# Kernel optimization log

Hardware: AMD Instinct MI355X
Metric: run time of the kernel (lower is better)

The kernel has to match this reference:

```python
import jax, jax.numpy as jnp
import numpy as np

WINDOW_SIZE = 11
SIGMA = 1.5
CHANNELS = 3
DATA_RANGE = 1.0


def _create_window(window_size, channel):
    x = np.arange(window_size) - window_size // 2
    g = np.exp(-(x ** 2) / (2.0 * SIGMA ** 2))
    g = g / g.sum()
    w2d = np.outer(g, g).astype(np.float32)  # [ws, ws]
    # depthwise kernel, OIHW with I=1, O=channel
    return jnp.asarray(np.broadcast_to(w2d, (channel, 1, window_size, window_size)).copy())


def _depthwise_conv(x, window, channel):
    # x: [B, C, H, W], window: [C, 1, ws, ws], VALID padding, groups=C
    return jax.lax.conv_general_dilated(
        x, window, window_strides=(1, 1), padding='VALID',
        dimension_numbers=('NCHW', 'OIHW', 'NCHW'),
        feature_group_count=channel)


def setup_inputs() -> dict:
    key = jax.random.key(0)
    k1, k2 = jax.random.split(key)
    img1 = jax.random.uniform(k1, (32, CHANNELS, 512, 512), dtype=jnp.float32)
    img2 = jax.random.uniform(k2, (32, CHANNELS, 512, 512), dtype=jnp.float32)
    return {"img1": img1, "img2": img2}


def reference(img1, img2):
    channel = img1.shape[1]
    window = _create_window(WINDOW_SIZE, channel).astype(img1.dtype)

    mu1 = _depthwise_conv(img1, window, channel)
    mu2 = _depthwise_conv(img2, window, channel)
    mu1_sq = mu1 * mu1
    mu2_sq = mu2 * mu2
    mu1_mu2 = mu1 * mu2

    sigma1_sq = _depthwise_conv(img1 * img1, window, channel) - mu1_sq
    sigma2_sq = _depthwise_conv(img2 * img2, window, channel) - mu2_sq
    sigma12 = _depthwise_conv(img1 * img2, window, channel) - mu1_mu2

    C1 = (0.01 * DATA_RANGE) ** 2
    C2 = (0.03 * DATA_RANGE) ** 2
    v1 = 2.0 * sigma12 + C2
    v2 = sigma1_sq + sigma2_sq + C2
    ssim_map = (2.0 * mu1_mu2 + C1) * v1 / ((mu1_sq + mu2_sq + C1) * v2)
    # mean over channel, height, width -> per-image SSIM [B]
    return ssim_map.mean(axis=(1, 2, 3))
```

## Files before the change

kernel.cpp:

```cpp
#include <hip/hip_runtime.h>
#include <math.h>

#define H 512
#define W 512
#define OUT_H 502
#define OUT_W 502
#define C1c 1.0e-4f
#define C2c 9.0e-4f

#define TH 56
#define NR (TH + 10)
#define NCOLS 256
#define HALO 10

__global__ __launch_bounds__(256, 4) void ssim_kernel(const float* __restrict__ img1,
                                                      const float* __restrict__ img2,
                                                      float* __restrict__ out) {
    __shared__ float2 ring[2][NCOLS + HALO];
    __shared__ float wsum[4];

    const int tid = threadIdx.x;

    float g[11];
    {
        float s = 0.f;
#pragma unroll
        for (int i = 0; i < 11; ++i) {
            float d = (float)(i - 5);
            g[i] = expf(-d * d * (1.0f / 4.5f));
            s += g[i];
        }
        float inv = 1.0f / s;
#pragma unroll
        for (int i = 0; i < 11; ++i) g[i] *= inv;
    }

    const int X0 = blockIdx.x * NCOLS;
    const int Y0 = blockIdx.y * TH;
    const int plane = blockIdx.z;
    const size_t pbase = (size_t)plane * (H * W);
    const float* __restrict__ p1 = img1 + pbase;
    const float* __restrict__ p2 = img2 + pbase;

    const int gx = X0 + tid;
    const int hx = min(X0 + NCOLS + tid, W - 1);

    float acc0[11], acc1[11], acc2[11], acc3[11], acc4[11];
#pragma unroll
    for (int i = 0; i < 11; ++i) { acc0[i]=0.f; acc1[i]=0.f; acc2[i]=0.f; acc3[i]=0.f; acc4[i]=0.f; }

    float lsum = 0.f;

    {
        const size_t rowoff = (size_t)min(Y0, H - 1) * W;
    }
    int gy0 = min(Y0, H - 1);
    float a1 = p1[(size_t)gy0 * W + gx];
    float a2 = p2[(size_t)gy0 * W + gx];
    float b1 = 0.f, b2 = 0.f;
    if (tid < HALO) { b1 = p1[(size_t)gy0 * W + hx]; b2 = p2[(size_t)gy0 * W + hx]; }

#pragma unroll 1
    for (int rb = 0; rb < NR; rb += 11) {
#pragma unroll
        for (int p = 0; p < 11; ++p) {
            const int r = rb + p;
            const int slot = r & 1;

            ring[slot][tid] = make_float2(a1, a2);
            if (tid < HALO) ring[slot][NCOLS + tid] = make_float2(b1, b2);

            {
                const int gy = min(Y0 + r + 1, H - 1);
                const size_t rowoff = (size_t)gy * W;
                a1 = p1[rowoff + gx];
                a2 = p2[rowoff + gx];
                if (tid < HALO) { b1 = p1[rowoff + hx]; b2 = p2[rowoff + hx]; }
            }

            __syncthreads();

            float h0 = 0.f, h1 = 0.f, h2 = 0.f, h3 = 0.f, h4 = 0.f;
            const float2* rp = &ring[slot][tid];
#pragma unroll
            for (int t = 0; t < 11; ++t) {
                const float2 v = rp[t];
                const float w = g[t];
                h0 = fmaf(w, v.x,       h0);
                h1 = fmaf(w, v.y,       h1);
                h2 = fmaf(w, v.x * v.x, h2);
                h3 = fmaf(w, v.y * v.y, h3);
                h4 = fmaf(w, v.x * v.y, h4);
            }

#pragma unroll
            for (int a = 0; a < 11; ++a) {
                const float w = g[(p - a + 11) % 11];
                acc0[a] = fmaf(w, h0, acc0[a]);
                acc1[a] = fmaf(w, h1, acc1[a]);
                acc2[a] = fmaf(w, h2, acc2[a]);
                acc3[a] = fmaf(w, h3, acc3[a]);
                acc4[a] = fmaf(w, h4, acc4[a]);
            }

            const int e = (p + 1) % 11;
            if (r >= 10) {
                const int oy = Y0 + r - 10;
                const float m1 = acc0[e], m2 = acc1[e];
                const float m1s = m1 * m1, m2s = m2 * m2, m12 = m1 * m2;
                const float sig1  = acc2[e] - m1s;
                const float sig2  = acc3[e] - m2s;
                const float sig12 = acc4[e] - m12;
                const float num = (2.f * m12 + C1c) * (2.f * sig12 + C2c);
                const float den = (m1s + m2s + C1c) * (sig1 + sig2 + C2c);
                const float v = num * __builtin_amdgcn_rcpf(den);
                if (gx < OUT_W && oy < OUT_H) lsum += v;
            }
            acc0[e] = 0.f; acc1[e] = 0.f; acc2[e] = 0.f; acc3[e] = 0.f; acc4[e] = 0.f;
        }
    }

#pragma unroll
    for (int off = 32; off > 0; off >>= 1) lsum += __shfl_down(lsum, off, 64);
    if ((tid & 63) == 0) wsum[tid >> 6] = lsum;
    __syncthreads();
    if (tid == 0) {
        const float inv_count = 1.0f / (3.0f * (float)OUT_H * (float)OUT_W);
        const float total = (wsum[0] + wsum[1] + wsum[2] + wsum[3]) * inv_count;
        atomicAdd(&out[plane / 3], total);
    }
}

__global__ void zero_out(float* out, int n) {
    int i = threadIdx.x + blockIdx.x * blockDim.x;
    if (i < n) out[i] = 0.f;
}

extern "C" void kernel_launch(void* const* d_in, const int* in_sizes, int n_in,
                              void* d_out, int out_size, void* d_ws, size_t ws_size,
                              hipStream_t stream) {
    const float* img1 = (const float*)d_in[0];
    const float* img2 = (const float*)d_in[1];
    float* out = (float*)d_out;

    zero_out<<<1, 64, 0, stream>>>(out, out_size);

    const int nplanes = in_sizes[0] / (H * W);
    dim3 grid(W / NCOLS,
              (OUT_H + TH - 1) / TH,
              nplanes);
    ssim_kernel<<<grid, 256, 0, stream>>>(img1, img2, out);
}
```

Baseline: 262.3 us.

## Give each wavefront a private 64-column ring, replacing block barriers with wave barriers

```diff
diff --git a/kernel.cpp b/kernel.cpp
--- a/kernel.cpp
+++ b/kernel.cpp
@@ -1,64 +1,58 @@
 #include <hip/hip_runtime.h>
-#include <math.h>
 
 #define H 512
 #define W 512
-#define OUT_H 502
-#define OUT_W 502
+#define OUT_Wc 502
+#define OUT_Hc 502
 #define C1c 1.0e-4f
 #define C2c 9.0e-4f
 
 #define TH 56
-#define NR (TH + 10)
-#define NCOLS 256
+#define NR 66
 #define HALO 10
+#define RSTRIDE 74
 
-__global__ __launch_bounds__(256, 4) void ssim_kernel(const float* __restrict__ img1,
+__global__ __launch_bounds__(256, 5) void ssim_kernel(const float* __restrict__ img1,
                                                       const float* __restrict__ img2,
                                                       float* __restrict__ out) {
-    __shared__ float2 ring[2][NCOLS + HALO];
-    __shared__ float wsum[4];
+    __shared__ float2 ring[4][2][RSTRIDE];
 
-    const int tid = threadIdx.x;
+    constexpr float GW[11] = {0.00102838f, 0.00759876f, 0.03600078f, 0.10936067f,
+                              0.21300555f, 0.26601174f, 0.21300555f, 0.10936067f,
+                              0.03600078f, 0.00759876f, 0.00102838f};
 
-    float g[11];
-    {
-        float s = 0.f;
-#pragma unroll
-        for (int i = 0; i < 11; ++i) {
-            float d = (float)(i - 5);
-            g[i] = expf(-d * d * (1.0f / 4.5f));
-            s += g[i];
-        }
-        float inv = 1.0f / s;
-#pragma unroll
-        for (int i = 0; i < 11; ++i) g[i] *= inv;
-    }
+    const int tid  = threadIdx.x;
+    const int wv   = tid >> 6;
+    const int lane = tid & 63;
 
-    const int X0 = blockIdx.x * NCOLS;
-    const int Y0 = blockIdx.y * TH;
     const int plane = blockIdx.z;
     const size_t pbase = (size_t)plane * (H * W);
     const float* __restrict__ p1 = img1 + pbase;
     const float* __restrict__ p2 = img2 + pbase;
 
-    const int gx = X0 + tid;
-    const int hx = min(X0 + NCOLS + tid, W - 1);
+    const int Y0    = blockIdx.y * TH;
+    const int wcol0 = (blockIdx.x * 4 + wv) * 64;
+    const int gx    = wcol0 + lane;
+    const int hx    = min(wcol0 + 64 + lane, W - 1);
+
+    float2 (* __restrict__ wring)[RSTRIDE] = ring[wv];
 
     float acc0[11], acc1[11], acc2[11], acc3[11], acc4[11];
 #pragma unroll
     for (int i = 0; i < 11; ++i) { acc0[i]=0.f; acc1[i]=0.f; acc2[i]=0.f; acc3[i]=0.f; acc4[i]=0.f; }
 
+    const bool colok = (gx < OUT_Wc);
     float lsum = 0.f;
 
     {
-        const size_t rowoff = (size_t)min(Y0, H - 1) * W;
+        const float* r1 = p1 + (size_t)Y0 * W;
+        const float* r2 = p2 + (size_t)Y0 * W;
     }
-    int gy0 = min(Y0, H - 1);
-    float a1 = p1[(size_t)gy0 * W + gx];
-    float a2 = p2[(size_t)gy0 * W + gx];
+    const float* r1p = p1 + (size_t)Y0 * W;
+    const float* r2p = p2 + (size_t)Y0 * W;
+    float a1 = r1p[gx], a2 = r2p[gx];
     float b1 = 0.f, b2 = 0.f;
-    if (tid < HALO) { b1 = p1[(size_t)gy0 * W + hx]; b2 = p2[(size_t)gy0 * W + hx]; }
+    if (lane < HALO) { b1 = r1p[hx]; b2 = r2p[hx]; }
 
 #pragma unroll 1
     for (int rb = 0; rb < NR; rb += 11) {
@@ -67,67 +61,76 @@
             const int r = rb + p;
             const int slot = r & 1;
 
-            ring[slot][tid] = make_float2(a1, a2);
-            if (tid < HALO) ring[slot][NCOLS + tid] = make_float2(b1, b2);
+            wring[slot][lane] = make_float2(a1, a2);
 
-            {
-                const int gy = min(Y0 + r + 1, H - 1);
-                const size_t rowoff = (size_t)gy * W;
-                a1 = p1[rowoff + gx];
-                a2 = p2[rowoff + gx];
-                if (tid < HALO) { b1 = p1[rowoff + hx]; b2 = p2[rowoff + hx]; }
+            const int gy = min(Y0 + r + 1, H - 1);
+            const float* __restrict__ n1 = p1 + (size_t)gy * W;
+            const float* __restrict__ n2 = p2 + (size_t)gy * W;
+
+            if (lane < HALO) {
+                wring[slot][64 + lane] = make_float2(b1, b2);
+                b1 = n1[hx]; b2 = n2[hx];
             }
+            a1 = n1[gx]; a2 = n2[gx];
 
-            __syncthreads();
+            __builtin_amdgcn_wave_barrier();
 
-            float h0 = 0.f, h1 = 0.f, h2 = 0.f, h3 = 0.f, h4 = 0.f;
-            const float2* rp = &ring[slot][tid];
+            float h0, h1, h2, h3, h4;
 #pragma unroll
             for (int t = 0; t < 11; ++t) {
-                const float2 v = rp[t];
-                const float w = g[t];
-                h0 = fmaf(w, v.x,       h0);
-                h1 = fmaf(w, v.y,       h1);
-                h2 = fmaf(w, v.x * v.x, h2);
-                h3 = fmaf(w, v.y * v.y, h3);
-                h4 = fmaf(w, v.x * v.y, h4);
+                const float2 v = wring[slot][lane + t];
+                const float w = GW[t];
+                if (t == 0) {
+                    h0 = w * v.x;         h1 = w * v.y;
+                    h2 = w * (v.x * v.x); h3 = w * (v.y * v.y);
+                    h4 = w * (v.x * v.y);
+                } else {
+                    h0 = fmaf(w, v.x,       h0);
+                    h1 = fmaf(w, v.y,       h1);
+                    h2 = fmaf(w, v.x * v.x, h2);
+                    h3 = fmaf(w, v.y * v.y, h3);
+                    h4 = fmaf(w, v.x * v.y, h4);
+                }
             }
 
 #pragma unroll
             for (int a = 0; a < 11; ++a) {
-                const float w = g[(p - a + 11) % 11];
-                acc0[a] = fmaf(w, h0, acc0[a]);
-                acc1[a] = fmaf(w, h1, acc1[a]);
-                acc2[a] = fmaf(w, h2, acc2[a]);
-                acc3[a] = fmaf(w, h3, acc3[a]);
-                acc4[a] = fmaf(w, h4, acc4[a]);
+                const float w = GW[(p - a + 11) % 11];
+                if (a == p) {
+                    acc0[a] = w * h0; acc1[a] = w * h1; acc2[a] = w * h2;
+                    acc3[a] = w * h3; acc4[a] = w * h4;
+                } else {
+                    acc0[a] = fmaf(w, h0, acc0[a]);
+                    acc1[a] = fmaf(w, h1, acc1[a]);
+                    acc2[a] = fmaf(w, h2, acc2[a]);
+                    acc3[a] = fmaf(w, h3, acc3[a]);
+                    acc4[a] = fmaf(w, h4, acc4[a]);
+                }
             }
 
             const int e = (p + 1) % 11;
-            if (r >= 10) {
-                const int oy = Y0 + r - 10;
+            const int oy = Y0 + r - 10;
+            if (r >= 10 && oy < OUT_Hc) {
                 const float m1 = acc0[e], m2 = acc1[e];
-                const float m1s = m1 * m1, m2s = m2 * m2, m12 = m1 * m2;
-                const float sig1  = acc2[e] - m1s;
-                const float sig2  = acc3[e] - m2s;
-                const float sig12 = acc4[e] - m12;
-                const float num = (2.f * m12 + C1c) * (2.f * sig12 + C2c);
-                const float den = (m1s + m2s + C1c) * (sig1 + sig2 + C2c);
-                const float v = num * __builtin_amdgcn_rcpf(den);
-                if (gx < OUT_W && oy < OUT_H) lsum += v;
+                const float m12 = m1 * m2;
+                const float sig1  = fmaf(-m1, m1, acc2[e]);
+                const float sig2  = fmaf(-m2, m2, acc3[e]);
+                const float sig12 = fmaf(-m1, m2, acc4[e]);
+                const float num_a = fmaf(2.f, m12,   C1c);
+                const float num_b = fmaf(2.f, sig12, C2c);
+                const float den_a = fmaf(m1, m1, fmaf(m2, m2, C1c));
+                const float den_b = (sig1 + sig2) + C2c;
+                const float v = (num_a * num_b) * __builtin_amdgcn_rcpf(den_a * den_b);
+                lsum += colok ? v : 0.f;
             }
-            acc0[e] = 0.f; acc1[e] = 0.f; acc2[e] = 0.f; acc3[e] = 0.f; acc4[e] = 0.f;
         }
     }
 
 #pragma unroll
     for (int off = 32; off > 0; off >>= 1) lsum += __shfl_down(lsum, off, 64);
-    if ((tid & 63) == 0) wsum[tid >> 6] = lsum;
-    __syncthreads();
-    if (tid == 0) {
-        const float inv_count = 1.0f / (3.0f * (float)OUT_H * (float)OUT_W);
-        const float total = (wsum[0] + wsum[1] + wsum[2] + wsum[3]) * inv_count;
-        atomicAdd(&out[plane / 3], total);
+    if (lane == 0) {
+        const float inv_count = 1.0f / (3.0f * (float)OUT_Hc * (float)OUT_Wc);
+        atomicAdd(&out[plane / 3], lsum * inv_count);
     }
 }
 
@@ -146,8 +149,8 @@
     zero_out<<<1, 64, 0, stream>>>(out, out_size);
 
     const int nplanes = in_sizes[0] / (H * W);
-    dim3 grid(W / NCOLS,
-              (OUT_H + TH - 1) / TH,
+    dim3 grid(2,
+              (OUT_Hc + TH - 1) / TH,
               nplanes);
     ssim_kernel<<<grid, 256, 0, stream>>>(img1, img2, out);
 }
```

Result: slower. 283.2 us (+8.0%).
